# Kernel optimization log

Measured on AMD Instinct MI355X. Metric: run time of the kernel, lower is better.

## Reference

```python
import jax, jax.numpy as jnp
import numpy as np

N = 50000      # nodes
E = 800000     # edges (avg degree 16)
D = 128        # embed_dim
H = 8          # nhead
HD = D // H    # head dim = 16


def setup_inputs() -> dict:
    key = jax.random.key(0)
    ks = jax.random.split(key, 6)
    s = 1.0 / np.sqrt(D)  # ~xavier scale for square matrices
    return {
        "feats": jax.random.normal(ks[0], (N, D), jnp.float32),
        "edge_index": jax.random.randint(ks[1], (E, 2), 0, N, dtype=jnp.int64),
        "Wq": jax.random.normal(ks[2], (D, D), jnp.float32) * s,
        "bq": jnp.zeros((D,), jnp.float32),
        "Wk": jax.random.normal(ks[3], (D, D), jnp.float32) * s,
        "bk": jnp.zeros((D,), jnp.float32),
        "Wv": jax.random.normal(ks[4], (D, D), jnp.float32) * s,
        "bv": jnp.zeros((D,), jnp.float32),
        "Wo": jax.random.normal(ks[5], (D, D), jnp.float32) * s,
        "bo": jnp.zeros((D,), jnp.float32),
    }


def reference(feats, edge_index, Wq, bq, Wk, bk, Wv, bv, Wo, bo):
    # Projections (nn.Linear: x @ W.T + b), split into heads: [N, H, HD]
    q = (feats @ Wq.T + bq).reshape(N, H, HD)
    k = (feats @ Wk.T + bk).reshape(N, H, HD)
    v = (feats @ Wv.T + bv).reshape(N, H, HD)

    r = edge_index[:, 0]  # source nodes
    c = edge_index[:, 1]  # destination nodes (softmax / aggregation groups)

    # Per-edge, per-head dot-product scores: [E, H]
    scores = jnp.einsum('ehd,ehd->eh', q[c], k[r]) / np.sqrt(HD)

    # Custom scatter-softmax: src_max clamped to min 0; extra exp(-src_max) in denom
    smax = jnp.maximum(jax.ops.segment_max(scores, c, num_segments=N), 0.0)  # [N, H]
    ex = jnp.exp(scores - smax[c])                                           # [E, H]
    denom = jax.ops.segment_sum(ex, c, num_segments=N)                       # [N, H]
    attn = ex / (denom + jnp.exp(-smax))[c]                                  # [E, H]

    # Weighted V per edge, scatter-mean to destination nodes
    out_e = attn[:, :, None] * v[r]                      # [E, H, HD]
    agg = jax.ops.segment_sum(out_e, c, num_segments=N)  # [N, H, HD]
    cnt = jax.ops.segment_sum(jnp.ones((E,), jnp.float32), c, num_segments=N)
    agg = agg / jnp.maximum(cnt, 1.0)[:, None, None]

    return agg.reshape(N, D) @ Wo.T + bo
```

## Files before the change

kernel.cpp:

```cpp
#include <hip/hip_runtime.h>
#include <hip/hip_bf16.h>

#define N_NODES 50000
#define N_EDGES 800000
#define DIM 128
#define NHEAD 8
#define HDIM 16
#define ELL_PAD 64

#define Q_OFF      0ull
#define KV_OFF     25600000ull
#define AGG_OFF    51200000ull
#define ELL_OFF    64000000ull
#define WBF_OFF    76800000ull
#define BIAS_OFF   76931072ull
#define CNT_OFF    76933376ull

typedef __attribute__((ext_vector_type(8))) short short8;
typedef __attribute__((ext_vector_type(4))) float floatx4;

__device__ inline float bflo2f(unsigned u) { return __uint_as_float(u << 16); }
__device__ inline float bfhi2f(unsigned u) { return __uint_as_float(u & 0xffff0000u); }
__device__ inline float2 unp2(unsigned u) {
    return make_float2(__uint_as_float(u << 16), __uint_as_float(u & 0xffff0000u));
}
__device__ inline void fma2(float2& a, float2 b, float2 c) {
    a.x = fmaf(b.x, c.x, a.x); a.y = fmaf(b.y, c.y, a.y);
}
__device__ inline unsigned short f2bf(float f) {
    unsigned u = __float_as_uint(f);
    return (unsigned short)((u + 0x7fffu + ((u >> 16) & 1u)) >> 16);
}

__device__ inline void detect_flags(const void* feats, const void* edge,
                                    int& isbf, int& is32) {
    const unsigned short* f = (const unsigned short*)feats;
    const unsigned int* eg = (const unsigned int*)edge;
    int lane = threadIdx.x & 63;
    unsigned e = (f[lane] >> 7) & 0xFF;
    int junk = (e >= 0x90 || (e > 0 && e <= 0x60)) ? 1 : 0;
    unsigned long long jm = __ballot(junk);
    int nz = (lane < 32 && eg[2 * lane + 1] != 0) ? 1 : 0;
    unsigned long long nm = __ballot(nz);
    isbf = (jm == 0ull) ? 1 : 0;
    is32 = (nm != 0ull) ? 1 : 0;
}

__device__ inline void load_edge(const int* edge, int is32, int e, int& r, int& c) {
    if (is32) { r = edge[2 * e]; c = edge[2 * e + 1]; }
    else {
        const long long* p = (const long long*)edge;
        r = (int)p[2 * e]; c = (int)p[2 * e + 1];
    }
    if ((unsigned)r >= N_NODES) r = 0;
    if ((unsigned)c >= N_NODES) c = 0;
}

__global__ __launch_bounds__(256) void prep_wb(const void* feats, const int* edge,
                                               const void* wq, const void* wk,
                                               const void* wv, const void* wo,
                                               const void* bq, const void* bk,
                                               const void* bv, const void* bo,
                                               unsigned short* wbf, float* bias) {
    int isbf, is32; detect_flags(feats, edge, isbf, is32);
    int b = blockIdx.x, t = threadIdx.x;
    if (b == 256) {
        for (int j = t; j < 512; j += 256) {
            int m2 = j >> 7, c2 = j & 127;
            const void* bb = (m2 == 0) ? bq : (m2 == 1) ? bk : (m2 == 2) ? bv : bo;
            bias[j] = isbf ? __bfloat162float(((const __hip_bfloat16*)bb)[c2])
                           : ((const float*)bb)[c2];
        }
        return;
    }
    if (isbf) return;
    int idx = b * 256 + t;
    int m = idx >> 14, rem = idx & 16383;
    const void* w = (m == 0) ? wq : (m == 1) ? wk : (m == 2) ? wv : wo;
    wbf[idx] = f2bf(((const float*)w)[rem]);
}

__global__ __launch_bounds__(256) void ell_build(const void* feats, const int* edge,
                                                 int* cnt, int* ell) {
    int isbf, is32; detect_flags(feats, edge, isbf, is32);
    int e = blockIdx.x * 256 + threadIdx.x;
    if (e >= N_EDGES) return;
    int r, c; load_edge(edge, is32, e, r, c);
    int slot = atomicAdd(cnt + c, 1);
    if (slot < ELL_PAD) ell[c * ELL_PAD + slot] = r;
}

__global__ __launch_bounds__(256) void qkv_mfma(const void* feats_raw, const int* edge,
                                                const void* wq_raw, const void* wk_raw,
                                                const void* wv_raw, const unsigned short* wbf,
                                                const float* bias,
                                                float* q, unsigned int* kvpack) {
    int isbf, is32; detect_flags(feats_raw, edge, isbf, is32);
    const unsigned short* W[3];
    W[0] = isbf ? (const unsigned short*)wq_raw : wbf;
    W[1] = isbf ? (const unsigned short*)wk_raw : wbf + 16384;
    W[2] = isbf ? (const unsigned short*)wv_raw : wbf + 32768;

    int wave = threadIdx.x >> 6, lane = threadIdx.x & 63;
    int rbase = blockIdx.x * 64 + wave * 16;
    int mrow = lane & 15, quad = lane >> 4;
    int arow = rbase + mrow; if (arow >= N_NODES) arow = N_NODES - 1;

    short8 a[4];
    if (isbf) {
        const unsigned short* ap = (const unsigned short*)feats_raw + (size_t)arow * DIM + quad * 8;
        #pragma unroll
        for (int kt = 0; kt < 4; ++kt) a[kt] = *(const short8*)(ap + kt * 32);
    } else {
        const float* af = (const float*)feats_raw + (size_t)arow * DIM + quad * 8;
        #pragma unroll
        for (int kt = 0; kt < 4; ++kt) {
            float4 f0 = *(const float4*)(af + kt * 32);
            float4 f1 = *(const float4*)(af + kt * 32 + 4);
            a[kt][0] = (short)f2bf(f0.x); a[kt][1] = (short)f2bf(f0.y);
            a[kt][2] = (short)f2bf(f0.z); a[kt][3] = (short)f2bf(f0.w);
            a[kt][4] = (short)f2bf(f1.x); a[kt][5] = (short)f2bf(f1.y);
            a[kt][6] = (short)f2bf(f1.z); a[kt][7] = (short)f2bf(f1.w);
        }
    }

    for (int m = 0; m < 3; ++m) {
        const unsigned short* wm = W[m];
        for (int nt = 0; nt < 8; ++nt) {
            const unsigned short* wp = wm + (size_t)(nt * 16 + mrow) * DIM + quad * 8;
            float b = bias[m * 128 + nt * 16 + mrow];
            floatx4 acc = {b, b, b, b};
            #pragma unroll
            for (int kt = 0; kt < 4; ++kt) {
                short8 bf = *(const short8*)(wp + kt * 32);
                acc = __builtin_amdgcn_mfma_f32_16x16x32_bf16(a[kt], bf, acc, 0, 0, 0);
            }
            if (m == 0) {
                #pragma unroll
                for (int r4 = 0; r4 < 4; ++r4) {
                    int row = rbase + quad * 4 + r4;
                    if (row < N_NODES) q[(size_t)row * DIM + nt * 16 + mrow] = acc[r4];
                }
            } else {
                int sel = (m == 2) ? 8 : 0;
                #pragma unroll
                for (int r4 = 0; r4 < 4; ++r4) {
                    float other = __shfl_xor(acc[r4], 1);
                    int row = rbase + quad * 4 + r4;
                    if (((lane & 1) == 0) && row < N_NODES) {
                        unsigned packed = (unsigned)f2bf(acc[r4]) | ((unsigned)f2bf(other) << 16);
                        kvpack[(size_t)row * 128 + nt * 16 + sel + (mrow >> 1)] = packed;
                    }
                }
            }
        }
    }
}

__global__ __launch_bounds__(256) void node_agg(const int* cnt, const int* ell,
                                                const float* q, const uint4* kvpack,
                                                uint4* agg_bf) {
    int node = (blockIdx.x * 256 + threadIdx.x) >> 6;
    int lane = threadIdx.x & 63;
    if (node >= N_NODES) return;
    int e = lane >> 3, h = lane & 7;

    float2 qv[8];
    const float4* qp = (const float4*)(q + (size_t)node * DIM + h * HDIM);
    #pragma unroll
    for (int i = 0; i < 4; ++i) {
        float4 tq = qp[i];
        qv[2 * i] = make_float2(tq.x, tq.y);
        qv[2 * i + 1] = make_float2(tq.z, tq.w);
    }

    int degt = cnt[node];
    int deg = degt < ELL_PAD ? degt : ELL_PAD;
    float l = 0.f;
    float2 acc[8];
    #pragma unroll
    for (int i = 0; i < 8; ++i) acc[i] = make_float2(0.f, 0.f);

    const int* erow = ell + node * ELL_PAD;
    for (int i0 = 0; i0 < deg; i0 += 8) {
        int idx = i0 + e;
        bool ok = idx < deg;
        int r = ok ? erow[idx] : 0;
        const uint4* kp = kvpack + (size_t)r * 32 + h * 4;
        uint4 ka = kp[0], kb = kp[1], va = kp[2], vb = kp[3];
        float2 s2 = make_float2(0.f, 0.f);
        fma2(s2, unp2(ka.x), qv[0]);
        fma2(s2, unp2(ka.y), qv[1]);
        fma2(s2, unp2(ka.z), qv[2]);
        fma2(s2, unp2(ka.w), qv[3]);
        fma2(s2, unp2(kb.x), qv[4]);
        fma2(s2, unp2(kb.y), qv[5]);
        fma2(s2, unp2(kb.z), qv[6]);
        fma2(s2, unp2(kb.w), qv[7]);
        float s = s2.x + s2.y;
        float p = ok ? __expf(s * 0.25f) : 0.f;
        l += p;
        float2 p2 = make_float2(p, p);
        fma2(acc[0], p2, unp2(va.x));
        fma2(acc[1], p2, unp2(va.y));
        fma2(acc[2], p2, unp2(va.z));
        fma2(acc[3], p2, unp2(va.w));
        fma2(acc[4], p2, unp2(vb.x));
        fma2(acc[5], p2, unp2(vb.y));
        fma2(acc[6], p2, unp2(vb.z));
        fma2(acc[7], p2, unp2(vb.w));
    }

    #pragma unroll
    for (int m = 8; m < 64; m <<= 1) {
        l += __shfl_xor(l, m);
        #pragma unroll
        for (int i = 0; i < 8; ++i) {
            acc[i].x += __shfl_xor(acc[i].x, m);
            acc[i].y += __shfl_xor(acc[i].y, m);
        }
    }

    float inv = 1.0f / ((1.0f + l) * (float)(degt > 0 ? degt : 1));
    if (e == 0) {
        unsigned o[8];
        #pragma unroll
        for (int i = 0; i < 8; ++i)
            o[i] = (unsigned)f2bf(acc[i].x * inv) | ((unsigned)f2bf(acc[i].y * inv) << 16);
        uint4* op = agg_bf + (size_t)node * 16 + h * 2;
        op[0] = make_uint4(o[0], o[1], o[2], o[3]);
        op[1] = make_uint4(o[4], o[5], o[6], o[7]);
    }
}

__global__ __launch_bounds__(256) void out_mfma(const unsigned short* agg_bf,
                                                const void* feats, const int* edge,
                                                const void* wo_raw, const unsigned short* wbf,
                                                const float* bias, void* out) {
    int isbf, is32; detect_flags(feats, edge, isbf, is32);
    const unsigned short* W = isbf ? (const unsigned short*)wo_raw : wbf + 49152;
    int wave = threadIdx.x >> 6, lane = threadIdx.x & 63;
    int rbase = blockIdx.x * 64 + wave * 16;
    int mrow = lane & 15, quad = lane >> 4;
    int arow = rbase + mrow; if (arow >= N_NODES) arow = N_NODES - 1;

    short8 a[4];
    const unsigned short* ap = agg_bf + (size_t)arow * DIM + quad * 8;
    #pragma unroll
    for (int kt = 0; kt < 4; ++kt) a[kt] = *(const short8*)(ap + kt * 32);

    for (int nt = 0; nt < 8; ++nt) {
        const unsigned short* wp = W + (size_t)(nt * 16 + mrow) * DIM + quad * 8;
        float b = bias[3 * 128 + nt * 16 + mrow];
        floatx4 acc = {b, b, b, b};
        #pragma unroll
        for (int kt = 0; kt < 4; ++kt) {
            short8 bf = *(const short8*)(wp + kt * 32);
            acc = __builtin_amdgcn_mfma_f32_16x16x32_bf16(a[kt], bf, acc, 0, 0, 0);
        }
        if (isbf) {
            #pragma unroll
            for (int r4 = 0; r4 < 4; ++r4) {
                float other = __shfl_xor(acc[r4], 1);
                int row = rbase + quad * 4 + r4;
                if (((lane & 1) == 0) && row < N_NODES) {
                    unsigned packed = (unsigned)f2bf(acc[r4]) | ((unsigned)f2bf(other) << 16);
                    int c = nt * 16 + mrow;
                    ((unsigned int*)out)[(size_t)row * 64 + (c >> 1)] = packed;
                }
            }
        } else {
            #pragma unroll
            for (int r4 = 0; r4 < 4; ++r4) {
                int row = rbase + quad * 4 + r4;
                if (row < N_NODES) ((float*)out)[(size_t)row * DIM + nt * 16 + mrow] = acc[r4];
            }
        }
    }
}

extern "C" void kernel_launch(void* const* d_in, const int* in_sizes, int n_in,
                              void* d_out, int out_size, void* d_ws, size_t ws_size,
                              hipStream_t stream) {
    const void* feats = d_in[0];
    const int*  edge  = (const int*)d_in[1];
    const void* Wq = d_in[2]; const void* bq = d_in[3];
    const void* Wk = d_in[4]; const void* bk = d_in[5];
    const void* Wv = d_in[6]; const void* bv = d_in[7];
    const void* Wo = d_in[8]; const void* bo = d_in[9];

    char* ws = (char*)d_ws;
    float* q             = (float*)(ws + Q_OFF);
    unsigned int* kvpack = (unsigned int*)(ws + KV_OFF);
    unsigned short* aggb = (unsigned short*)(ws + AGG_OFF);
    int* ell             = (int*)(ws + ELL_OFF);
    unsigned short* wbf  = (unsigned short*)(ws + WBF_OFF);
    float* bias          = (float*)(ws + BIAS_OFF);
    int* cnt             = (int*)(ws + CNT_OFF);

    hipMemsetAsync(ws + CNT_OFF, 0, N_NODES * 4, stream);

    prep_wb<<<257, 256, 0, stream>>>(feats, edge, Wq, Wk, Wv, Wo, bq, bk, bv, bo,
                                     wbf, bias);

    ell_build<<<(N_EDGES + 255) / 256, 256, 0, stream>>>(feats, edge, cnt, ell);

    qkv_mfma<<<(N_NODES + 63) / 64, 256, 0, stream>>>(feats, edge, Wq, Wk, Wv, wbf,
                                                      bias, q, kvpack);

    node_agg<<<(N_NODES * 64 + 255) / 256, 256, 0, stream>>>(cnt, ell, q,
                                                             (const uint4*)kvpack,
                                                             (uint4*)aggb);

    out_mfma<<<(N_NODES + 63) / 64, 256, 0, stream>>>(aggb, feats, edge, Wo, wbf,
                                                      bias, d_out);
}
```

Baseline: 292.4 us.

## Fold count reset into prep kernel, batch edges in ELL build, unroll aggregation

The separate memset of the per-node counters is removed and the zeroing is done inside the prep_wb kernel, which saves a launch. ell_build now handles two edges per thread with half as many blocks. node_agg processes two neighbor edges per lane per iteration to raise memory-level parallelism for the K/V gathers, and switches to scalar float accumulators with __restrict__ pointers. The cost is more registers in node_agg and fewer threads issuing atomics in ell_build.

```diff
diff --git a/kernel.cpp b/kernel.cpp
--- a/kernel.cpp
+++ b/kernel.cpp
@@ -21,12 +21,6 @@
 
 __device__ inline float bflo2f(unsigned u) { return __uint_as_float(u << 16); }
 __device__ inline float bfhi2f(unsigned u) { return __uint_as_float(u & 0xffff0000u); }
-__device__ inline float2 unp2(unsigned u) {
-    return make_float2(__uint_as_float(u << 16), __uint_as_float(u & 0xffff0000u));
-}
-__device__ inline void fma2(float2& a, float2 b, float2 c) {
-    a.x = fmaf(b.x, c.x, a.x); a.y = fmaf(b.y, c.y, a.y);
-}
 __device__ inline unsigned short f2bf(float f) {
     unsigned u = __float_as_uint(f);
     return (unsigned short)((u + 0x7fffu + ((u >> 16) & 1u)) >> 16);
@@ -61,9 +55,13 @@
                                                const void* wv, const void* wo,
                                                const void* bq, const void* bk,
                                                const void* bv, const void* bo,
-                                               unsigned short* wbf, float* bias) {
+                                               unsigned short* wbf, float* bias, int* cnt) {
     int isbf, is32; detect_flags(feats, edge, isbf, is32);
     int b = blockIdx.x, t = threadIdx.x;
+    if (b < 196) {
+        int i = b * 256 + t;
+        if (i < N_NODES) cnt[i] = 0;
+    }
     if (b == 256) {
         for (int j = t; j < 512; j += 256) {
             int m2 = j >> 7, c2 = j & 127;
@@ -83,11 +81,15 @@
 __global__ __launch_bounds__(256) void ell_build(const void* feats, const int* edge,
                                                  int* cnt, int* ell) {
     int isbf, is32; detect_flags(feats, edge, isbf, is32);
-    int e = blockIdx.x * 256 + threadIdx.x;
-    if (e >= N_EDGES) return;
-    int r, c; load_edge(edge, is32, e, r, c);
-    int slot = atomicAdd(cnt + c, 1);
-    if (slot < ELL_PAD) ell[c * ELL_PAD + slot] = r;
+    int e0 = (blockIdx.x * 256 + threadIdx.x) * 2;
+    #pragma unroll
+    for (int j = 0; j < 2; ++j) {
+        int e = e0 + j;
+        if (e >= N_EDGES) return;
+        int r, c; load_edge(edge, is32, e, r, c);
+        int slot = atomicAdd(cnt + c, 1);
+        if (slot < ELL_PAD) ell[c * ELL_PAD + slot] = r;
+    }
 }
 
 __global__ __launch_bounds__(256) void qkv_mfma(const void* feats_raw, const int* edge,
@@ -157,68 +159,88 @@
     }
 }
 
-__global__ __launch_bounds__(256) void node_agg(const int* cnt, const int* ell,
-                                                const float* q, const uint4* kvpack,
-                                                uint4* agg_bf) {
+__global__ __launch_bounds__(256) void node_agg(const int* __restrict__ cnt,
+                                                const int* __restrict__ ell,
+                                                const float* __restrict__ q,
+                                                const uint4* __restrict__ kvpack,
+                                                uint4* __restrict__ agg_bf) {
     int node = (blockIdx.x * 256 + threadIdx.x) >> 6;
     int lane = threadIdx.x & 63;
     if (node >= N_NODES) return;
     int e = lane >> 3, h = lane & 7;
 
-    float2 qv[8];
+    float qv[16];
     const float4* qp = (const float4*)(q + (size_t)node * DIM + h * HDIM);
     #pragma unroll
     for (int i = 0; i < 4; ++i) {
         float4 tq = qp[i];
-        qv[2 * i] = make_float2(tq.x, tq.y);
-        qv[2 * i + 1] = make_float2(tq.z, tq.w);
+        qv[4 * i] = tq.x; qv[4 * i + 1] = tq.y; qv[4 * i + 2] = tq.z; qv[4 * i + 3] = tq.w;
     }
 
     int degt = cnt[node];
     int deg = degt < ELL_PAD ? degt : ELL_PAD;
     float l = 0.f;
-    float2 acc[8];
-    #pragma unroll
-    for (int i = 0; i < 8; ++i) acc[i] = make_float2(0.f, 0.f);
+    float acc[16];
+    #pragma unroll
+    for (int i = 0; i < 16; ++i) acc[i] = 0.f;
 
     const int* erow = ell + node * ELL_PAD;
-    for (int i0 = 0; i0 < deg; i0 += 8) {
-        int idx = i0 + e;
-        bool ok = idx < deg;
-        int r = ok ? erow[idx] : 0;
-        const uint4* kp = kvpack + (size_t)r * 32 + h * 4;
-        uint4 ka = kp[0], kb = kp[1], va = kp[2], vb = kp[3];
-        float2 s2 = make_float2(0.f, 0.f);
-        fma2(s2, unp2(ka.x), qv[0]);
-        fma2(s2, unp2(ka.y), qv[1]);
-        fma2(s2, unp2(ka.z), qv[2]);
-        fma2(s2, unp2(ka.w), qv[3]);
-        fma2(s2, unp2(kb.x), qv[4]);
-        fma2(s2, unp2(kb.y), qv[5]);
-        fma2(s2, unp2(kb.z), qv[6]);
-        fma2(s2, unp2(kb.w), qv[7]);
-        float s = s2.x + s2.y;
-        float p = ok ? __expf(s * 0.25f) : 0.f;
-        l += p;
-        float2 p2 = make_float2(p, p);
-        fma2(acc[0], p2, unp2(va.x));
-        fma2(acc[1], p2, unp2(va.y));
-        fma2(acc[2], p2, unp2(va.z));
-        fma2(acc[3], p2, unp2(va.w));
-        fma2(acc[4], p2, unp2(vb.x));
-        fma2(acc[5], p2, unp2(vb.y));
-        fma2(acc[6], p2, unp2(vb.z));
-        fma2(acc[7], p2, unp2(vb.w));
+    for (int i0 = 0; i0 < deg; i0 += 16) {
+        int i1 = i0 + e, i2 = i0 + 8 + e;
+        bool ok1 = i1 < deg, ok2 = i2 < deg;
+        int r1 = ok1 ? erow[i1] : 0;
+        int r2 = ok2 ? erow[i2] : 0;
+        const uint4* kp1 = kvpack + (size_t)r1 * 32 + h * 4;
+        const uint4* kp2 = kvpack + (size_t)r2 * 32 + h * 4;
+        uint4 ka1 = kp1[0], kb1 = kp1[1], va1 = kp1[2], vb1 = kp1[3];
+        uint4 ka2 = kp2[0], kb2 = kp2[1], va2 = kp2[2], vb2 = kp2[3];
+
+        float s1 = 0.f;
+        s1 += bflo2f(ka1.x) * qv[0]  + bfhi2f(ka1.x) * qv[1];
+        s1 += bflo2f(ka1.y) * qv[2]  + bfhi2f(ka1.y) * qv[3];
+        s1 += bflo2f(ka1.z) * qv[4]  + bfhi2f(ka1.z) * qv[5];
+        s1 += bflo2f(ka1.w) * qv[6]  + bfhi2f(ka1.w) * qv[7];
+        s1 += bflo2f(kb1.x) * qv[8]  + bfhi2f(kb1.x) * qv[9];
+        s1 += bflo2f(kb1.y) * qv[10] + bfhi2f(kb1.y) * qv[11];
+        s1 += bflo2f(kb1.z) * qv[12] + bfhi2f(kb1.z) * qv[13];
+        s1 += bflo2f(kb1.w) * qv[14] + bfhi2f(kb1.w) * qv[15];
+        float p1 = ok1 ? __expf(s1 * 0.25f) : 0.f;
+        l += p1;
+        acc[0]  += p1 * bflo2f(va1.x); acc[1]  += p1 * bfhi2f(va1.x);
+        acc[2]  += p1 * bflo2f(va1.y); acc[3]  += p1 * bfhi2f(va1.y);
+        acc[4]  += p1 * bflo2f(va1.z); acc[5]  += p1 * bfhi2f(va1.z);
+        acc[6]  += p1 * bflo2f(va1.w); acc[7]  += p1 * bfhi2f(va1.w);
+        acc[8]  += p1 * bflo2f(vb1.x); acc[9]  += p1 * bfhi2f(vb1.x);
+        acc[10] += p1 * bflo2f(vb1.y); acc[11] += p1 * bfhi2f(vb1.y);
+        acc[12] += p1 * bflo2f(vb1.z); acc[13] += p1 * bfhi2f(vb1.z);
+        acc[14] += p1 * bflo2f(vb1.w); acc[15] += p1 * bfhi2f(vb1.w);
+
+        float s2 = 0.f;
+        s2 += bflo2f(ka2.x) * qv[0]  + bfhi2f(ka2.x) * qv[1];
+        s2 += bflo2f(ka2.y) * qv[2]  + bfhi2f(ka2.y) * qv[3];
+        s2 += bflo2f(ka2.z) * qv[4]  + bfhi2f(ka2.z) * qv[5];
+        s2 += bflo2f(ka2.w) * qv[6]  + bfhi2f(ka2.w) * qv[7];
+        s2 += bflo2f(kb2.x) * qv[8]  + bfhi2f(kb2.x) * qv[9];
+        s2 += bflo2f(kb2.y) * qv[10] + bfhi2f(kb2.y) * qv[11];
+        s2 += bflo2f(kb2.z) * qv[12] + bfhi2f(kb2.z) * qv[13];
+        s2 += bflo2f(kb2.w) * qv[14] + bfhi2f(kb2.w) * qv[15];
+        float p2 = ok2 ? __expf(s2 * 0.25f) : 0.f;
+        l += p2;
+        acc[0]  += p2 * bflo2f(va2.x); acc[1]  += p2 * bfhi2f(va2.x);
+        acc[2]  += p2 * bflo2f(va2.y); acc[3]  += p2 * bfhi2f(va2.y);
+        acc[4]  += p2 * bflo2f(va2.z); acc[5]  += p2 * bfhi2f(va2.z);
+        acc[6]  += p2 * bflo2f(va2.w); acc[7]  += p2 * bfhi2f(va2.w);
+        acc[8]  += p2 * bflo2f(vb2.x); acc[9]  += p2 * bfhi2f(vb2.x);
+        acc[10] += p2 * bflo2f(vb2.y); acc[11] += p2 * bfhi2f(vb2.y);
+        acc[12] += p2 * bflo2f(vb2.z); acc[13] += p2 * bfhi2f(vb2.z);
+        acc[14] += p2 * bflo2f(vb2.w); acc[15] += p2 * bfhi2f(vb2.w);
     }
 
     #pragma unroll
     for (int m = 8; m < 64; m <<= 1) {
         l += __shfl_xor(l, m);
         #pragma unroll
-        for (int i = 0; i < 8; ++i) {
-            acc[i].x += __shfl_xor(acc[i].x, m);
-            acc[i].y += __shfl_xor(acc[i].y, m);
-        }
+        for (int i = 0; i < 16; ++i) acc[i] += __shfl_xor(acc[i], m);
     }
 
     float inv = 1.0f / ((1.0f + l) * (float)(degt > 0 ? degt : 1));
@@ -226,7 +248,7 @@
         unsigned o[8];
         #pragma unroll
         for (int i = 0; i < 8; ++i)
-            o[i] = (unsigned)f2bf(acc[i].x * inv) | ((unsigned)f2bf(acc[i].y * inv) << 16);
+            o[i] = (unsigned)f2bf(acc[2 * i] * inv) | ((unsigned)f2bf(acc[2 * i + 1] * inv) << 16);
         uint4* op = agg_bf + (size_t)node * 16 + h * 2;
         op[0] = make_uint4(o[0], o[1], o[2], o[3]);
         op[1] = make_uint4(o[4], o[5], o[6], o[7]);
@@ -298,12 +320,10 @@
     float* bias          = (float*)(ws + BIAS_OFF);
     int* cnt             = (int*)(ws + CNT_OFF);
 
-    hipMemsetAsync(ws + CNT_OFF, 0, N_NODES * 4, stream);
-
     prep_wb<<<257, 256, 0, stream>>>(feats, edge, Wq, Wk, Wv, Wo, bq, bk, bv, bo,
-                                     wbf, bias);
-
-    ell_build<<<(N_EDGES + 255) / 256, 256, 0, stream>>>(feats, edge, cnt, ell);
+                                     wbf, bias, cnt);
+
+    ell_build<<<(N_EDGES / 2 + 255) / 256, 256, 0, stream>>>(feats, edge, cnt, ell);
 
     qkv_mfma<<<(N_NODES + 63) / 64, 256, 0, stream>>>(feats, edge, Wq, Wk, Wv, wbf,
                                                       bias, q, kvpack);
```

Measured after the change: 287.8 us. Within noise of the previous version (-1.5%).
